# Kernel optimization log

Hardware: AMD Instinct MI355X
Metric: run time of the kernel (lower is better)

The kernel has to match this reference:

```python
import jax, jax.numpy as jnp
import numpy as np

B, D, L, H, W, T = 256, 512, 32, 14, 14, 8


def _lin(x, w, b=None):
    y = x @ w.T
    return y if b is None else y + b


def _conv1x1(x, w, b):  # x: [B,C,H,W], w: [O,C], b: [O]
    return jnp.einsum('oc,bchw->bohw', w, x) + b[None, :, None, None]


def setup_inputs() -> dict:
    key = jax.random.key(0)
    ks = jax.random.split(key, 24)
    s = 0.02
    inp = {
        'c': jax.random.normal(ks[0], (B, D), jnp.float32),
        'm': jax.random.normal(ks[1], (B, D), jnp.float32),
        'k': jax.random.normal(ks[2], (B, D, H, W), jnp.float32),
        'q': jax.random.normal(ks[3], (B, D), jnp.float32),
        'cw': jax.random.normal(ks[4], (B, L, D), jnp.float32),
        'mask': jax.random.randint(ks[5], (B, L), 0, 2, jnp.int32),
        'cs': jax.random.normal(ks[6], (T, B, D), jnp.float32),
        'ms': jax.random.normal(ks[7], (T, B, D), jnp.float32),
        # ControlUnit params
        'Wcq': jax.random.normal(ks[8], (D, 2 * D), jnp.float32) * s,
        'bcq': jnp.zeros((D,), jnp.float32),
        'Wca': jax.random.normal(ks[9], (1, D), jnp.float32) * s,
        'bca': jnp.zeros((1,), jnp.float32),
        # ReadUnit params
        'Wm_r': jax.random.normal(ks[10], (D, D), jnp.float32) * s,
        'bm_r': jnp.zeros((D,), jnp.float32),
        'Wk': jax.random.normal(ks[11], (D, D), jnp.float32) * s,
        'bk': jnp.zeros((D,), jnp.float32),
        'WI': jax.random.normal(ks[12], (D, 2 * D), jnp.float32) * s,
        'bI': jnp.zeros((D,), jnp.float32),
        'Wra': jax.random.normal(ks[13], (D, D), jnp.float32) * s,
        'bra': jnp.zeros((D,), jnp.float32),
        # WriteUnit params
        'Wm_w': jax.random.normal(ks[14], (D, 2 * D), jnp.float32) * s,
        'bm_w': jnp.zeros((D,), jnp.float32),
        'Wsa': jax.random.normal(ks[15], (1, D), jnp.float32) * s,
        'bsa': jnp.zeros((1,), jnp.float32),
        'Wm2': jax.random.normal(ks[16], (D, D), jnp.float32) * s,
        'bm2': jnp.zeros((D,), jnp.float32),
        'Wc': jax.random.normal(ks[17], (1, D), jnp.float32) * s,
        'bc': jnp.ones((1,), jnp.float32),  # linear_c.bias.data.fill_(1)
        'Ws': jax.random.normal(ks[18], (D, D), jnp.float32) * s,
    }
    return inp


def reference(c, m, k, q, cw, mask, cs, ms,
              Wcq, bcq, Wca, bca,
              Wm_r, bm_r, Wk, bk, WI, bI, Wra, bra,
              Wm_w, bm_w, Wsa, bsa, Wm2, bm2, Wc, bc, Ws):
    # ---- ControlUnit ----
    cq = _lin(jnp.concatenate([c, q], axis=1), Wcq, bcq)          # [B,D]
    ca = _lin(cq[:, None, :] * cw, Wca, bca)                      # [B,L,1]
    ca = jnp.where(mask[:, :, None] > 0, ca, -jnp.inf)            # mask padding
    cv = jax.nn.softmax(ca, axis=1)                               # [B,L,1]
    c_new = jnp.sum(cv * cw, axis=1)                              # [B,D]

    # ---- ReadUnit ----
    mI = _lin(m, Wm_r, bm_r)                                      # [B,D]
    I = mI[:, :, None, None] * _conv1x1(k, Wk, bk)                # [B,D,H,W]
    I_ = _conv1x1(jnp.concatenate([I, k], axis=1), WI, bI)        # [B,D,H,W]
    ra = _conv1x1(I_ * c_new[:, :, None, None], Wra, bra)         # [B,D,H,W]
    rv = jax.nn.softmax(ra, axis=1)                               # Softmax2d = over channels
    r = jnp.sum(rv * k, axis=(-1, -2))                            # [B,D]

    # ---- WriteUnit ----
    m_prev = _lin(jnp.concatenate([r, m], axis=1), Wm_w, bm_w)    # [B,D]
    m_ = _lin(m_prev, Wm2, bm2)                                   # [B,D]
    gate = jax.nn.sigmoid(_lin(c_new, Wc, bc))                    # [B,1]
    sa = jax.nn.softmax(_lin(cs * gate[None, :, :], Wsa, bsa), axis=0)  # [T,B,1]
    m_sa = jnp.sum(sa * ms, axis=0)                               # [B,D]
    m_ = m_ + m_sa @ Ws.T
    m_new = gate * m + (1.0 - gate) * m_                          # [B,D]

    return (c_new, m_new, cv, rv)
```

## Files before the change

kernel.cpp:

```cpp
#include <hip/hip_runtime.h>
#include <hip/hip_bf16.h>

#define BB 256
#define DD 512
#define LL 32
#define HWN 196
#define TT 8
#define STEPB 12544

typedef __hip_bfloat16 bf16;
typedef __attribute__((ext_vector_type(8))) short short8;
typedef __attribute__((ext_vector_type(4))) float f32x4;

__device__ __forceinline__ float b2f(bf16 x) { return __bfloat162float(x); }
__device__ __forceinline__ unsigned short f2bu(float x) {
    bf16 h = __float2bfloat16(x);
    return *(unsigned short*)&h;
}
#define NEG_INF (-__builtin_huge_valf())

__device__ __forceinline__ void gload_lds16(const void* g, void* l) {
    __builtin_amdgcn_global_load_lds(
        (const __attribute__((address_space(1))) void*)g,
        (__attribute__((address_space(3))) void*)l, 16, 0, 0);
}
__device__ __forceinline__ void gload_lds4(const void* g, void* l) {
    __builtin_amdgcn_global_load_lds(
        (const __attribute__((address_space(1))) void*)g,
        (__attribute__((address_space(3))) void*)l, 4, 0, 0);
}

__global__ __launch_bounds__(256) void cvt_w_kernel(
    const float* __restrict__ src, unsigned short* __restrict__ dst, int n4)
{
    int i = blockIdx.x*256 + threadIdx.x;
    if (i < n4) {
        float4 f = ((const float4*)src)[i];
        ushort4 u;
        u.x = f2bu(f.x); u.y = f2bu(f.y); u.z = f2bu(f.z); u.w = f2bu(f.w);
        ((ushort4*)dst)[i] = u;
    }
}

__global__ __launch_bounds__(256) void pack_x_kernel(
    const float* __restrict__ X, char* __restrict__ Xp)
{
    int b = blockIdx.x, s = blockIdx.y;
    uint2* chunk = (uint2*)(Xp + ((size_t)(b*16 + s))*STEPB);
    for (int idx = threadIdx.x; idx < 8*49; idx += 256) {
        int kq = idx / 49, n4 = idx % 49;
        const float* p = X + ((size_t)b*DD + s*32 + kq*4)*HWN + n4*4;
        ushort4 r[4];
        #pragma unroll
        for (int i = 0; i < 4; ++i) {
            float4 f = *(const float4*)(p + (size_t)i*HWN);
            r[i].x = f2bu(f.x); r[i].y = f2bu(f.y); r[i].z = f2bu(f.z); r[i].w = f2bu(f.w);
        }
        uint2* cell = chunk + kq*196 + n4*4;
        *(uint4*)(cell) = make_uint4(
            (uint)r[0].x | ((uint)r[1].x << 16), (uint)r[2].x | ((uint)r[3].x << 16),
            (uint)r[0].y | ((uint)r[1].y << 16), (uint)r[2].y | ((uint)r[3].y << 16));
        *(uint4*)(cell + 2) = make_uint4(
            (uint)r[0].z | ((uint)r[1].z << 16), (uint)r[2].z | ((uint)r[3].z << 16),
            (uint)r[0].w | ((uint)r[1].w << 16), (uint)r[2].w | ((uint)r[3].w << 16));
    }
}

__global__ __launch_bounds__(256) void small_gemm_kernel(
    const float* __restrict__ A1, int K1,
    const float* __restrict__ A2, int K2,
    const float* __restrict__ Wt, const float* __restrict__ bias,
    float* __restrict__ outf, int Dout)
{
    __shared__ float xs[1024];
    int b = blockIdx.x, tid = threadIdx.x;
    int K = K1 + K2;
    for (int i = tid; i < K; i += 256) {
        xs[i] = (i < K1) ? A1[(size_t)b*K1 + i] : A2[(size_t)b*K2 + (i - K1)];
    }
    __syncthreads();
    for (int d = tid; d < Dout; d += 256) {
        const float4* wrow = (const float4*)(Wt + (size_t)d * K);
        float acc = 0.f;
        for (int j = 0; j < K/4; ++j) {
            float4 w = wrow[j];
            acc += w.x*xs[j*4] + w.y*xs[j*4+1] + w.z*xs[j*4+2] + w.w*xs[j*4+3];
        }
        if (bias) acc += bias[d];
        outf[(size_t)b*Dout + d] = acc;
    }
}

__global__ __launch_bounds__(256) void control_kernel(
    const float* __restrict__ cq, const float* __restrict__ cw,
    const float* __restrict__ Wca, const float* __restrict__ bca,
    const int* __restrict__ mask,
    float* __restrict__ cnew_f, float* __restrict__ cv_out, float* __restrict__ cnew_out)
{
    __shared__ float u[DD];
    __shared__ float cas[LL];
    __shared__ float cvs[LL];
    int b = blockIdx.x, tid = threadIdx.x;
    for (int d = tid; d < DD; d += 256) u[d] = cq[(size_t)b*DD + d] * Wca[d];
    __syncthreads();
    int wave = tid >> 6, lane = tid & 63;
    float bca0 = bca[0];
    for (int lw = 0; lw < 8; ++lw) {
        int l = wave*8 + lw;
        const float4* w4 = (const float4*)(cw + ((size_t)(b*LL + l))*DD + lane*8);
        float4 wa = w4[0], wb = w4[1];
        const float* uu = &u[lane*8];
        float p = wa.x*uu[0] + wa.y*uu[1] + wa.z*uu[2] + wa.w*uu[3]
                + wb.x*uu[4] + wb.y*uu[5] + wb.z*uu[6] + wb.w*uu[7];
        for (int off = 32; off > 0; off >>= 1) p += __shfl_down(p, off);
        if (lane == 0) {
            float v = p + bca0;
            if (mask[b*LL + l] <= 0) v = NEG_INF;
            cas[l] = v;
        }
    }
    __syncthreads();
    if (tid < LL) {
        float mx = NEG_INF;
        for (int j = 0; j < LL; ++j) mx = fmaxf(mx, cas[j]);
        float s = 0.f;
        for (int j = 0; j < LL; ++j) s += __expf(cas[j] - mx);
        float cv = __expf(cas[tid] - mx) / s;
        cvs[tid] = cv;
        cv_out[b*LL + tid] = cv;
    }
    __syncthreads();
    for (int d = tid; d < DD; d += 256) {
        float acc = 0.f;
        for (int l = 0; l < LL; ++l) acc += cvs[l] * cw[((size_t)(b*LL + l))*DD + d];
        cnew_f[(size_t)b*DD + d] = acc;
        cnew_out[(size_t)b*DD + d] = acc;
    }
}

__global__ __launch_bounds__(512) void conv_mfma_kernel(
    const char* __restrict__ X1p, int ns1,
    const char* __restrict__ X2p, int ns2,
    const unsigned short* __restrict__ Wb, int C,
    const float* __restrict__ bias, const float* __restrict__ oscale,
    void* __restrict__ Yout, int packed_out)
{
    __shared__ __align__(16) char Xs[2][12800];
    int b = blockIdx.x, ot = blockIdx.y;
    int tid = threadIdx.x;
    int wave = tid >> 6, lane = tid & 63;
    int wm = wave >> 1, wn = wave & 1;
    int obase = ot*128 + wm*32;
    int n0 = wn*112;
    int ntn = wn ? 6 : 7;
    int ln = lane & 15, lq = lane >> 4;

    auto STAGE = [&](int s, char* lb) {
        const char* chunk = (s < ns1) ? X1p + ((size_t)b*ns1 + s)*STEPB
                                      : X2p + ((size_t)b*ns2 + (s - ns1))*STEPB;
        for (int i = wave; i < 13; i += 8) {
            if (i < 12) gload_lds16(chunk + i*1024 + lane*16, lb + i*1024);
            else        gload_lds4 (chunk + 12288 + lane*4,  lb + 12288);
        }
    };

    f32x4 acc[2][7];
    #pragma unroll
    for (int mt = 0; mt < 2; ++mt)
        #pragma unroll
        for (int nt = 0; nt < 7; ++nt) acc[mt][nt] = (f32x4){0.f, 0.f, 0.f, 0.f};

    STAGE(0, Xs[0]);
    int nsteps = ns1 + ns2;
    for (int s = 0; s < nsteps; ++s) {
        char* cur = Xs[s & 1];
        char* nxt = Xs[(s & 1) ^ 1];
        __syncthreads();
        short8 a0 = *(const short8*)(Wb + (size_t)(obase + ln)*C + s*32 + lq*8);
        short8 a1 = *(const short8*)(Wb + (size_t)(obase + 16 + ln)*C + s*32 + lq*8);
        __builtin_amdgcn_sched_barrier(0);
        if (s + 1 < nsteps) STAGE(s + 1, nxt);
        const uint2* cells = (const uint2*)cur;
        #pragma unroll
        for (int nt = 0; nt < 7; ++nt) {
            if (nt < ntn) {
                int n = n0 + nt*16 + ln;
                uint2 c0 = cells[(lq*2)*196 + n];
                uint2 c1 = cells[(lq*2 + 1)*196 + n];
                union { uint4 u; short8 s8; } bb;
                bb.u = make_uint4(c0.x, c0.y, c1.x, c1.y);
                acc[0][nt] = __builtin_amdgcn_mfma_f32_16x16x32_bf16(a0, bb.s8, acc[0][nt], 0, 0, 0);
                acc[1][nt] = __builtin_amdgcn_mfma_f32_16x16x32_bf16(a1, bb.s8, acc[1][nt], 0, 0, 0);
            }
        }
    }
    if (packed_out) {
        uint2* Yp = (uint2*)Yout;
        #pragma unroll
        for (int mt = 0; mt < 2; ++mt) {
            int o4 = obase + mt*16 + lq*4;
            int st = o4 >> 5, kqo = (o4 & 31) >> 2;
            float bo[4], os[4];
            #pragma unroll
            for (int rr = 0; rr < 4; ++rr) {
                bo[rr] = bias[o4 + rr];
                os[rr] = oscale ? oscale[(size_t)b*DD + o4 + rr] : 1.f;
            }
            #pragma unroll
            for (int nt = 0; nt < 7; ++nt) {
                int hw = n0 + nt*16 + ln;
                if (nt < ntn && hw < HWN) {
                    unsigned short v[4];
                    #pragma unroll
                    for (int rr = 0; rr < 4; ++rr)
                        v[rr] = f2bu((acc[mt][nt][rr] + bo[rr]) * os[rr]);
                    Yp[((size_t)(b*16 + st)*8 + kqo)*196 + hw] =
                        make_uint2((uint)v[0] | ((uint)v[1] << 16),
                                   (uint)v[2] | ((uint)v[3] << 16));
                }
            }
        }
    } else {
        unsigned short* Y = (unsigned short*)Yout;
        #pragma unroll
        for (int mt = 0; mt < 2; ++mt) {
            #pragma unroll
            for (int rr = 0; rr < 4; ++rr) {
                int o = obase + mt*16 + lq*4 + rr;
                float bo = bias[o];
                float os = oscale ? oscale[(size_t)b*DD + o] : 1.f;
                #pragma unroll
                for (int nt = 0; nt < 7; ++nt) {
                    int hw = n0 + nt*16 + ln;
                    if (nt < ntn && hw < HWN) {
                        float v = (acc[mt][nt][rr] + bo) * os;
                        Y[((size_t)b*DD + o)*HWN + hw] = f2bu(v);
                    }
                }
            }
        }
    }
}

__global__ __launch_bounds__(512) void softmax_r_kernel(
    const bf16* __restrict__ ra, const float* __restrict__ kin,
    float* __restrict__ rv, float* __restrict__ r)
{
    __shared__ float pm[2][HWN], ps[2][HWN];
    __shared__ float mxs[HWN], sis[HWN];
    int b = blockIdx.x, tid = threadIdx.x;
    int half = tid >> 8, hw = tid & 255;
    if (hw < HWN) {
        float m = NEG_INF, s = 0.f;
        const bf16* base = ra + ((size_t)b*DD + half*256)*HWN + hw;
        for (int c = 0; c < 256; ++c) {
            float x = b2f(base[(size_t)c*HWN]);
            float nm = fmaxf(m, x);
            s = s*__expf(m - nm) + __expf(x - nm);
            m = nm;
        }
        pm[half][hw] = m; ps[half][hw] = s;
    }
    __syncthreads();
    if (tid < HWN) {
        float m0 = pm[0][tid], m1 = pm[1][tid];
        float m = fmaxf(m0, m1);
        float s = ps[0][tid]*__expf(m0 - m) + ps[1][tid]*__expf(m1 - m);
        mxs[tid] = m; sis[tid] = 1.f/s;
    }
    __syncthreads();
    int wave = tid >> 6, lane = tid & 63;
    for (int ci = 0; ci < 64; ++ci) {
        int c = wave*64 + ci;
        float psum = 0.f;
        #pragma unroll
        for (int g = 0; g < 4; ++g) {
            int hw2 = lane + 64*g;
            if (hw2 < HWN) {
                size_t idx = ((size_t)b*DD + c)*HWN + hw2;
                float e = __expf(b2f(ra[idx]) - mxs[hw2]) * sis[hw2];
                rv[idx] = e;
                psum += e * kin[idx];
            }
        }
        for (int off = 32; off > 0; off >>= 1) psum += __shfl_down(psum, off);
        if (lane == 0) r[(size_t)b*DD + c] = psum;
    }
}

__global__ __launch_bounds__(256) void samsa_kernel(
    const float* __restrict__ cs, const float* __restrict__ ms,
    const float* __restrict__ Wsa, const float* __restrict__ bsa,
    const float* __restrict__ cnew, const float* __restrict__ Wc, const float* __restrict__ bc,
    float* __restrict__ gate_out, float* __restrict__ msa)
{
    __shared__ float lg[TT];
    __shared__ float sas[TT];
    __shared__ float xw[DD];
    __shared__ float gsh;
    int b = blockIdx.x, tid = threadIdx.x;
    int wave = tid >> 6, lane = tid & 63;
    for (int d = tid; d < DD; d += 256) xw[d] = Wsa[d];
    __syncthreads();
    for (int tw = 0; tw < 2; ++tw) {
        int t = wave + 4*tw;
        const float4* c4 = (const float4*)(cs + ((size_t)t*BB + b)*DD + lane*8);
        float4 ca = c4[0], cb = c4[1];
        const float* ww = &xw[lane*8];
        float p = ca.x*ww[0] + ca.y*ww[1] + ca.z*ww[2] + ca.w*ww[3]
                + cb.x*ww[4] + cb.y*ww[5] + cb.z*ww[6] + cb.w*ww[7];
        for (int off = 32; off > 0; off >>= 1) p += __shfl_down(p, off);
        if (lane == 0) lg[t] = p;
    }
    if (wave == 0) {
        const float4* w4 = (const float4*)(Wc + lane*8);
        const float* x = &cnew[(size_t)b*DD + lane*8];
        float4 wa = w4[0], wb = w4[1];
        float p = wa.x*x[0] + wa.y*x[1] + wa.z*x[2] + wa.w*x[3]
                + wb.x*x[4] + wb.y*x[5] + wb.z*x[6] + wb.w*x[7];
        for (int off = 32; off > 0; off >>= 1) p += __shfl_down(p, off);
        if (lane == 0) {
            float g = 1.f / (1.f + __expf(-(p + bc[0])));
            gsh = g; gate_out[b] = g;
        }
    }
    __syncthreads();
    if (tid < TT) {
        float g = gsh, b0 = bsa[0];
        float mx = NEG_INF;
        for (int j = 0; j < TT; ++j) mx = fmaxf(mx, g*lg[j] + b0);
        float s = 0.f;
        for (int j = 0; j < TT; ++j) s += __expf(g*lg[j] + b0 - mx);
        sas[tid] = __expf(g*lg[tid] + b0 - mx) / s;
    }
    __syncthreads();
    for (int d = tid; d < DD; d += 256) {
        float acc = 0.f;
        for (int t = 0; t < TT; ++t) acc += sas[t] * ms[((size_t)t*BB + b)*DD + d];
        msa[(size_t)b*DD + d] = acc;
    }
}

__global__ __launch_bounds__(256) void write_final_kernel(
    const float* __restrict__ msa, const float* __restrict__ Ws,
    const float* __restrict__ m, const float* __restrict__ gate,
    const float* __restrict__ mund, float* __restrict__ mnew)
{
    __shared__ float xs[DD];
    int b = blockIdx.x, tid = threadIdx.x;
    for (int i = tid; i < DD; i += 256) xs[i] = msa[(size_t)b*DD + i];
    __syncthreads();
    float g = gate[b];
    for (int d = tid; d < DD; d += 256) {
        const float4* wrow = (const float4*)(Ws + (size_t)d * DD);
        float acc = 0.f;
        for (int j = 0; j < DD/4; ++j) {
            float4 w = wrow[j];
            acc += w.x*xs[j*4] + w.y*xs[j*4+1] + w.z*xs[j*4+2] + w.w*xs[j*4+3];
        }
        size_t idx = (size_t)b*DD + d;
        mnew[idx] = g * m[idx] + (1.f - g) * (mund[idx] + acc);
    }
}

extern "C" void kernel_launch(void* const* d_in, const int* in_sizes, int n_in,
                              void* d_out, int out_size, void* d_ws, size_t ws_size,
                              hipStream_t stream)
{
    (void)in_sizes; (void)n_in; (void)out_size; (void)ws_size;
    const float* c    = (const float*)d_in[0];
    const float* m    = (const float*)d_in[1];
    const float* k    = (const float*)d_in[2];
    const float* q    = (const float*)d_in[3];
    const float* cw   = (const float*)d_in[4];
    const int*   mask = (const int*)  d_in[5];
    const float* cs   = (const float*)d_in[6];
    const float* ms   = (const float*)d_in[7];
    const float* Wcq  = (const float*)d_in[8];
    const float* bcq  = (const float*)d_in[9];
    const float* Wca  = (const float*)d_in[10];
    const float* bca  = (const float*)d_in[11];
    const float* Wm_r = (const float*)d_in[12];
    const float* bm_r = (const float*)d_in[13];
    const float* Wk   = (const float*)d_in[14];
    const float* bk   = (const float*)d_in[15];
    const float* WI   = (const float*)d_in[16];
    const float* bI   = (const float*)d_in[17];
    const float* Wra  = (const float*)d_in[18];
    const float* bra  = (const float*)d_in[19];
    const float* Wm_w = (const float*)d_in[20];
    const float* bm_w = (const float*)d_in[21];
    const float* Wsa  = (const float*)d_in[22];
    const float* bsa  = (const float*)d_in[23];
    const float* Wm2  = (const float*)d_in[24];
    const float* bm2  = (const float*)d_in[25];
    const float* Wc   = (const float*)d_in[26];
    const float* bc   = (const float*)d_in[27];
    const float* Ws   = (const float*)d_in[28];

    float* out_cnew = (float*)d_out;
    float* out_mnew = out_cnew + BB*DD;
    float* out_cv   = out_mnew + BB*DD;
    float* out_rv   = out_cv + BB*LL;

    char* Ip  = (char*)out_rv;
    char* I2p = (char*)out_rv + 51380224;

    char* w = (char*)d_ws;
    float* s0      = (float*)(w + 0);
    float* s1      = (float*)(w + 524288);
    float* s2      = (float*)(w + 1048576);
    float* s3      = (float*)(w + 1572864);
    unsigned short* Wkb  = (unsigned short*)(w + 2097152);
    unsigned short* WIb  = (unsigned short*)(w + 2621440);
    unsigned short* Wrab = (unsigned short*)(w + 3670016);
    char* kp_ra = (char*)(w + 4194304);
    float* gate_w  = (float*)(w + 55574528);

    float* cq_w   = s0;
    float* r_w    = s0;
    float* cnew_w = s1;
    float* mI_w   = s2;
    float* mund_w = s2;
    float* mprev_w= s3;
    float* msa_w  = s3;
    unsigned short* ra_w = (unsigned short*)kp_ra;

    cvt_w_kernel<<<256, 256, 0, stream>>>(Wk,  Wkb,  65536);
    cvt_w_kernel<<<512, 256, 0, stream>>>(WI,  WIb,  131072);
    cvt_w_kernel<<<256, 256, 0, stream>>>(Wra, Wrab, 65536);

    pack_x_kernel<<<dim3(BB, 16), 256, 0, stream>>>(k, kp_ra);

    small_gemm_kernel<<<BB, 256, 0, stream>>>(c, DD, q, DD, Wcq, bcq, cq_w, DD);
    small_gemm_kernel<<<BB, 256, 0, stream>>>(m, DD, nullptr, 0, Wm_r, bm_r, mI_w, DD);
    control_kernel<<<BB, 256, 0, stream>>>(cq_w, cw, Wca, bca, mask, cnew_w, out_cv, out_cnew);

    conv_mfma_kernel<<<dim3(BB, 4), 512, 0, stream>>>(kp_ra, 16, nullptr, 0,  Wkb,  DD,   bk,  mI_w,   Ip,   1);
    conv_mfma_kernel<<<dim3(BB, 4), 512, 0, stream>>>(Ip,    16, kp_ra,  16,  WIb,  2*DD, bI,  cnew_w, I2p,  1);
    conv_mfma_kernel<<<dim3(BB, 4), 512, 0, stream>>>(I2p,   16, nullptr, 0,  Wrab, DD,   bra, nullptr, ra_w, 0);
    softmax_r_kernel<<<BB, 512, 0, stream>>>((const bf16*)ra_w, k, out_rv, r_w);

    small_gemm_kernel<<<BB, 256, 0, stream>>>(r_w, DD, m, DD, Wm_w, bm_w, mprev_w, DD);
    small_gemm_kernel<<<BB, 256, 0, stream>>>(mprev_w, DD, nullptr, 0, Wm2, bm2, mund_w, DD);
    samsa_kernel<<<BB, 256, 0, stream>>>(cs, ms, Wsa, bsa, cnew_w, Wc, bc, gate_w, msa_w);
    write_final_kernel<<<BB, 256, 0, stream>>>(msa_w, Ws, m, gate_w, mund_w, out_mnew);
}
```

Baseline: 791.8 us.

## Deepen conv MFMA pipeline to 4 LDS stages with hw-major packed layout

Changes the packed bf16 activation layout so each spatial position holds its 32 channels contiguously (64 bytes). B fragments become a single 16-byte LDS read instead of two 8-byte reads. The conv kernel moves from a double-buffered to a 4-buffer LDS ring, loading three stages ahead and prefetching weight fragments one step ahead. It uses explicit vmcnt waits and raw s_barrier to overlap global loads with MFMA work. The risks are more LDS per block, which may lower occupancy, a fragile hand-written waitcnt scheme, and possible LDS bank conflicts from the new 64-byte stride.

```diff
diff --git a/kernel.cpp b/kernel.cpp
--- a/kernel.cpp
+++ b/kernel.cpp
@@ -46,23 +46,17 @@
     const float* __restrict__ X, char* __restrict__ Xp)
 {
     int b = blockIdx.x, s = blockIdx.y;
-    uint2* chunk = (uint2*)(Xp + ((size_t)(b*16 + s))*STEPB);
-    for (int idx = threadIdx.x; idx < 8*49; idx += 256) {
-        int kq = idx / 49, n4 = idx % 49;
-        const float* p = X + ((size_t)b*DD + s*32 + kq*4)*HWN + n4*4;
-        ushort4 r[4];
-        #pragma unroll
-        for (int i = 0; i < 4; ++i) {
-            float4 f = *(const float4*)(p + (size_t)i*HWN);
-            r[i].x = f2bu(f.x); r[i].y = f2bu(f.y); r[i].z = f2bu(f.z); r[i].w = f2bu(f.w);
-        }
-        uint2* cell = chunk + kq*196 + n4*4;
-        *(uint4*)(cell) = make_uint4(
-            (uint)r[0].x | ((uint)r[1].x << 16), (uint)r[2].x | ((uint)r[3].x << 16),
-            (uint)r[0].y | ((uint)r[1].y << 16), (uint)r[2].y | ((uint)r[3].y << 16));
-        *(uint4*)(cell + 2) = make_uint4(
-            (uint)r[0].z | ((uint)r[1].z << 16), (uint)r[2].z | ((uint)r[3].z << 16),
-            (uint)r[0].w | ((uint)r[1].w << 16), (uint)r[2].w | ((uint)r[3].w << 16));
+    char* chunk = Xp + ((size_t)(b*16 + s))*STEPB;
+    for (int i = threadIdx.x; i < 4*HWN; i += 256) {
+        int n = i >> 2, kqp = i & 3;
+        const float* base = X + ((size_t)b*DD + s*32 + kqp*8)*HWN + n;
+        uint v[4];
+        #pragma unroll
+        for (int h = 0; h < 4; ++h) {
+            float f0 = base[(size_t)(2*h+0)*HWN], f1 = base[(size_t)(2*h+1)*HWN];
+            v[h] = (uint)f2bu(f0) | ((uint)f2bu(f1) << 16);
+        }
+        *(uint4*)(chunk + n*64 + kqp*16) = make_uint4(v[0], v[1], v[2], v[3]);
     }
 }
 
@@ -145,7 +139,7 @@
     const float* __restrict__ bias, const float* __restrict__ oscale,
     void* __restrict__ Yout, int packed_out)
 {
-    __shared__ __align__(16) char Xs[2][12800];
+    __shared__ __align__(16) char Xs[4][12800];
     int b = blockIdx.x, ot = blockIdx.y;
     int tid = threadIdx.x;
     int wave = tid >> 6, lane = tid & 63;
@@ -154,14 +148,19 @@
     int n0 = wn*112;
     int ntn = wn ? 6 : 7;
     int ln = lane & 15, lq = lane >> 4;
-
-    auto STAGE = [&](int s, char* lb) {
+    int nsteps = ns1 + ns2;
+
+    auto STAGE = [&](int s) {
         const char* chunk = (s < ns1) ? X1p + ((size_t)b*ns1 + s)*STEPB
                                       : X2p + ((size_t)b*ns2 + (s - ns1))*STEPB;
-        for (int i = wave; i < 13; i += 8) {
-            if (i < 12) gload_lds16(chunk + i*1024 + lane*16, lb + i*1024);
-            else        gload_lds4 (chunk + 12288 + lane*4,  lb + 12288);
-        }
+        char* lb = Xs[s & 3];
+        gload_lds16(chunk + wave*1024 + lane*16, lb + wave*1024);
+        if (wave < 5)       gload_lds16(chunk + (wave+8)*1024 + lane*16, lb + (wave+8)*1024);
+        else if (wave == 7) gload_lds4 (chunk + 12288 + lane*4, lb + 12288);
+    };
+    auto ALOAD = [&](int s, short8& a0, short8& a1) {
+        a0 = *(const short8*)(Wb + (size_t)(obase + ln)*C + s*32 + lq*8);
+        a1 = *(const short8*)(Wb + (size_t)(obase + 16 + ln)*C + s*32 + lq*8);
     };
 
     f32x4 acc[2][7];
@@ -170,36 +169,63 @@
         #pragma unroll
         for (int nt = 0; nt < 7; ++nt) acc[mt][nt] = (f32x4){0.f, 0.f, 0.f, 0.f};
 
-    STAGE(0, Xs[0]);
-    int nsteps = ns1 + ns2;
-    for (int s = 0; s < nsteps; ++s) {
-        char* cur = Xs[s & 1];
-        char* nxt = Xs[(s & 1) ^ 1];
-        __syncthreads();
-        short8 a0 = *(const short8*)(Wb + (size_t)(obase + ln)*C + s*32 + lq*8);
-        short8 a1 = *(const short8*)(Wb + (size_t)(obase + 16 + ln)*C + s*32 + lq*8);
-        __builtin_amdgcn_sched_barrier(0);
-        if (s + 1 < nsteps) STAGE(s + 1, nxt);
-        const uint2* cells = (const uint2*)cur;
+    short8 a0c, a1c, a0n, a1n;
+
+    STAGE(0);
+    STAGE(1);
+    __builtin_amdgcn_sched_barrier(0);
+    ALOAD(0, a0c, a1c);
+    __builtin_amdgcn_sched_barrier(0);
+    STAGE(2);
+
+    auto BODY = [&](int s, bool doA, bool doX) {
+        __builtin_amdgcn_s_barrier();
+        if (doA) ALOAD(s + 1, a0n, a1n);
+        __builtin_amdgcn_sched_barrier(0);
+        if (doX) STAGE(s + 3);
+        __builtin_amdgcn_sched_barrier(0);
+        const char* curb = Xs[s & 3];
         #pragma unroll
         for (int nt = 0; nt < 7; ++nt) {
             if (nt < ntn) {
                 int n = n0 + nt*16 + ln;
-                uint2 c0 = cells[(lq*2)*196 + n];
-                uint2 c1 = cells[(lq*2 + 1)*196 + n];
                 union { uint4 u; short8 s8; } bb;
-                bb.u = make_uint4(c0.x, c0.y, c1.x, c1.y);
-                acc[0][nt] = __builtin_amdgcn_mfma_f32_16x16x32_bf16(a0, bb.s8, acc[0][nt], 0, 0, 0);
-                acc[1][nt] = __builtin_amdgcn_mfma_f32_16x16x32_bf16(a1, bb.s8, acc[1][nt], 0, 0, 0);
+                bb.u = *(const uint4*)(curb + n*64 + lq*16);
+                acc[0][nt] = __builtin_amdgcn_mfma_f32_16x16x32_bf16(a0c, bb.s8, acc[0][nt], 0, 0, 0);
+                acc[1][nt] = __builtin_amdgcn_mfma_f32_16x16x32_bf16(a1c, bb.s8, acc[1][nt], 0, 0, 0);
             }
         }
-    }
+        a0c = a0n; a1c = a1n;
+    };
+
+    for (int s = 0; s <= nsteps - 4; ++s) {
+        asm volatile("s_waitcnt vmcnt(2)" ::: "memory");
+        __builtin_amdgcn_sched_barrier(0);
+        BODY(s, true, true);
+    }
+    {
+        asm volatile("s_waitcnt vmcnt(2)" ::: "memory");
+        __builtin_amdgcn_sched_barrier(0);
+        BODY(nsteps - 3, true, false);
+    }
+    {
+        asm volatile("s_waitcnt vmcnt(0)" ::: "memory");
+        __builtin_amdgcn_sched_barrier(0);
+        BODY(nsteps - 2, true, false);
+    }
+    {
+        asm volatile("s_waitcnt vmcnt(0)" ::: "memory");
+        __builtin_amdgcn_sched_barrier(0);
+        BODY(nsteps - 1, false, false);
+    }
+
     if (packed_out) {
         uint2* Yp = (uint2*)Yout;
         #pragma unroll
         for (int mt = 0; mt < 2; ++mt) {
             int o4 = obase + mt*16 + lq*4;
             int st = o4 >> 5, kqo = (o4 & 31) >> 2;
+            uint2* chunk = Yp + (size_t)(b*16 + st)*1568;
             float bo[4], os[4];
             #pragma unroll
             for (int rr = 0; rr < 4; ++rr) {
@@ -214,7 +240,7 @@
                     #pragma unroll
                     for (int rr = 0; rr < 4; ++rr)
                         v[rr] = f2bu((acc[mt][nt][rr] + bo[rr]) * os[rr]);
-                    Yp[((size_t)(b*16 + st)*8 + kqo)*196 + hw] =
+                    chunk[hw*8 + kqo] =
                         make_uint2((uint)v[0] | ((uint)v[1] << 16),
                                    (uint)v[2] | ((uint)v[3] << 16));
                 }
```

New measurement: 783.1 us. About the same (-1.1%).
